# Optimization experiments

Hardware: AMD Instinct MI355X
Metric: run time of the kernel (lower is better)

Reference implementation:

```python
import jax, jax.numpy as jnp
import numpy as np

NUM_HEADS = 8
OUT_CH = 64
IN_CH = 512
N_NODES = 65536


def setup_inputs() -> dict:
    key = jax.random.key(0)
    ks = jax.random.split(key, 8)
    s = 1.0 / np.sqrt(IN_CH)
    return {
        "query_input": jax.random.normal(ks[0], (N_NODES, IN_CH), jnp.float32),
        "source_input": jax.random.normal(ks[1], (N_NODES, IN_CH), jnp.float32),
        "Wq_w": jax.random.normal(ks[2], (NUM_HEADS * OUT_CH, IN_CH), jnp.float32) * s,
        "Wq_b": jax.random.normal(ks[3], (NUM_HEADS * OUT_CH,), jnp.float32) * s,
        "Wk_w": jax.random.normal(ks[4], (NUM_HEADS * OUT_CH, IN_CH), jnp.float32) * s,
        "Wk_b": jax.random.normal(ks[5], (NUM_HEADS * OUT_CH,), jnp.float32) * s,
        "Wv_w": jax.random.normal(ks[6], (NUM_HEADS * OUT_CH, IN_CH), jnp.float32) * s,
        "Wv_b": jax.random.normal(ks[7], (NUM_HEADS * OUT_CH,), jnp.float32) * s,
    }


def reference(query_input, source_input, Wq_w, Wq_b, Wk_w, Wk_b, Wv_w, Wv_b):
    N = query_input.shape[0]
    # Linear projections (torch nn.Linear: x @ W^T + b), reshape to [N, H, D]
    qs = (query_input @ Wq_w.T + Wq_b).reshape(N, NUM_HEADS, OUT_CH)
    ks = (source_input @ Wk_w.T + Wk_b).reshape(N, NUM_HEADS, OUT_CH)
    vs = (source_input @ Wv_w.T + Wv_b).reshape(N, NUM_HEADS, OUT_CH)
    # GLOBAL Frobenius-norm normalization (torch.norm with no dim)
    qs = qs / jnp.linalg.norm(qs)
    ks = ks / jnp.linalg.norm(ks)
    Nf = jnp.asarray(N, qs.dtype)
    # Global KV aggregation: [H, D, D]
    kvs = jnp.einsum('lhm,lhd->hmd', ks, vs)
    attention_num = jnp.einsum('nhm,hmd->nhd', qs, kvs) + Nf * vs
    ks_sum = ks.sum(axis=0)  # [H, D]
    attention_normalizer = jnp.einsum('nhm,hm->nh', qs, ks_sum)[..., None] + Nf
    attn_output = attention_num / attention_normalizer  # [N, H, D]
    return attn_output.mean(axis=1)  # [N, D]
```

## Files before the change

kernel.cpp:

```cpp
#include <hip/hip_runtime.h>
#include <stdint.h>

typedef __attribute__((ext_vector_type(8))) short short8;
typedef __attribute__((ext_vector_type(4))) float f32x4;

__device__ __forceinline__ uint32_t pk2bf(float a, float b) {
  uint32_t r;
  asm("v_cvt_pk_bf16_f32 %0, %1, %2" : "=v"(r) : "v"(a), "v"(b));
  return r;
}
__device__ __forceinline__ uint16_t f2bf(float a) {
  uint32_t ua = __builtin_bit_cast(uint32_t, a);
  return (uint16_t)((ua + 0x7FFFu + ((ua >> 16) & 1u)) >> 16);
}
__device__ __forceinline__ float bflo(uint32_t w) { return __builtin_bit_cast(float, w << 16); }
__device__ __forceinline__ float bfhi(uint32_t w) { return __builtin_bit_cast(float, w & 0xFFFF0000u); }

__device__ __forceinline__ void gload_lds16(const void* g, void* l) {
  __builtin_amdgcn_global_load_lds(
      (const __attribute__((address_space(1))) uint32_t*)g,
      (__attribute__((address_space(3))) uint32_t*)l, 16, 0, 0);
}

__global__ __launch_bounds__(256) void k_cvtw(const float* __restrict__ Wq,
                                              const float* __restrict__ Wk,
                                              const float* __restrict__ Wv,
                                              uint16_t* __restrict__ Wb) {
  const int idx = blockIdx.x * 256 + threadIdx.x;
  const int sel = idx >> 16;
  const int e = idx & 65535;
  const float* src = (sel == 0) ? Wq : (sel == 1) ? Wk : Wv;
  const float4 v = *(const float4*)(src + (size_t)e * 4);
  uint2 p;
  p.x = pk2bf(v.x, v.y);
  p.y = pk2bf(v.z, v.w);
  *(uint2*)(Wb + (size_t)sel * 262144 + (size_t)e * 4) = p;
}

__global__ __launch_bounds__(256, 2) void k_gemm_qkv(
    const float* __restrict__ qin, const float* __restrict__ sin_,
    const uint16_t* __restrict__ Wb,
    const float* __restrict__ bq, const float* __restrict__ bk,
    const float* __restrict__ bv,
    uint16_t* __restrict__ Qb, uint16_t* __restrict__ Kb, uint16_t* __restrict__ Vb,
    float* __restrict__ norms, float* __restrict__ ks_sum) {
  __shared__ float Asf[128 * 64];
  __shared__ uint16_t Bs[256 * 64];
  __shared__ float ksp[256];
  __shared__ float red[4];

  const int b0 = blockIdx.x;
  const int blk = (b0 & 7) * 384 + (b0 >> 3);
  const int rt = blk / 6, rem = blk % 6;
  const int proj = rem >> 1, ct = rem & 1;
  const int row0 = rt * 128, cb = ct * 256;

  const float* A = proj ? sin_ : qin;
  const uint16_t* W = Wb + (size_t)proj * 262144;
  const float* Bi = (proj == 0) ? bq : (proj == 1) ? bk : bv;
  uint16_t* O = (proj == 0) ? Qb : (proj == 1) ? Kb : Vb;

  const int tid = threadIdx.x;
  const int lane = tid & 63;
  const int wv = tid >> 6;
  const int wr = wv >> 1, wc = wv & 1;
  const int l15 = lane & 15, lhi = lane >> 4;

  f32x4 acc[4][8];
#pragma unroll
  for (int m = 0; m < 4; ++m)
#pragma unroll
    for (int n = 0; n < 8; ++n) acc[m][n] = (f32x4){0.f, 0.f, 0.f, 0.f};

  for (int kt = 0; kt < 8; ++kt) {
    const int k0 = kt * 64;
#pragma unroll
    for (int i = 0; i < 8; ++i) {
      const int arow = (wv * 8 + i) * 4 + (lane >> 4);
      const int ac16 = (lane & 15) ^ (arow & 7);
      gload_lds16(A + (size_t)(row0 + arow) * 512 + k0 + ac16 * 4,
                  &Asf[(wv * 8 + i) * 256]);
    }
#pragma unroll
    for (int i = 0; i < 8; ++i) {
      const int brow = (wv * 8 + i) * 8 + (lane >> 3);
      const int bc16 = (lane & 7) ^ (brow & 7);
      gload_lds16(W + (size_t)(cb + brow) * 512 + k0 + bc16 * 8,
                  &Bs[(wv * 8 + i) * 512]);
    }
    __syncthreads();
#pragma unroll
    for (int kk = 0; kk < 2; ++kk) {
      short8 a[4], b[8];
#pragma unroll
      for (int m = 0; m < 4; ++m) {
        const int r = wr * 64 + m * 16 + l15;
        const int base = r * 256 + kk * 128 + lhi * 32;
        const int sw = (r & 7) << 4;
        const f32x4 f0 = *(const f32x4*)((const char*)Asf + (base ^ sw));
        const f32x4 f1 = *(const f32x4*)((const char*)Asf + ((base + 16) ^ sw));
        uint32_t* ap = (uint32_t*)&a[m];
        ap[0] = pk2bf(f0[0], f0[1]);
        ap[1] = pk2bf(f0[2], f0[3]);
        ap[2] = pk2bf(f1[0], f1[1]);
        ap[3] = pk2bf(f1[2], f1[3]);
      }
#pragma unroll
      for (int n = 0; n < 8; ++n) {
        const int c = wc * 128 + n * 16 + l15;
        const int bo = (c * 128 + kk * 64 + lhi * 16) ^ ((c & 7) << 4);
        b[n] = *(const short8*)((const char*)Bs + bo);
      }
#pragma unroll
      for (int m = 0; m < 4; ++m)
#pragma unroll
        for (int n = 0; n < 8; ++n)
          acc[m][n] = __builtin_amdgcn_mfma_f32_16x16x32_bf16(a[m], b[n], acc[m][n], 0, 0, 0);
    }
    __syncthreads();
  }

  float nrm = 0.f;
  float cs[8];
#pragma unroll
  for (int n = 0; n < 8; ++n) cs[n] = 0.f;
#pragma unroll
  for (int n = 0; n < 8; ++n) {
    const int colg = cb + wc * 128 + n * 16 + l15;
    const float bias = Bi[colg];
#pragma unroll
    for (int m = 0; m < 4; ++m) {
      const int rowb = row0 + wr * 64 + m * 16 + lhi * 4;
#pragma unroll
      for (int r = 0; r < 4; ++r) {
        const float v = acc[m][n][r] + bias;
        O[(size_t)(rowb + r) * 512 + colg] = f2bf(v);
        nrm += v * v;
        cs[n] += v;
      }
    }
  }
#pragma unroll
  for (int o = 32; o >= 1; o >>= 1) nrm += __shfl_xor(nrm, o, 64);
  if (lane == 0) red[wv] = nrm;
  ksp[tid] = 0.f;
  __syncthreads();
  if (proj == 1) {
#pragma unroll
    for (int n = 0; n < 8; ++n) {
      cs[n] += __shfl_xor(cs[n], 16, 64);
      cs[n] += __shfl_xor(cs[n], 32, 64);
    }
    if (lhi == 0) {
#pragma unroll
      for (int n = 0; n < 8; ++n) atomicAdd(&ksp[wc * 128 + n * 16 + l15], cs[n]);
    }
  }
  __syncthreads();
  if (tid == 0 && proj < 2)
    atomicAdd(&norms[proj], red[0] + red[1] + red[2] + red[3]);
  if (proj == 1) atomicAdd(&ks_sum[cb + tid], ksp[tid]);
}

__global__ __launch_bounds__(512) void k_kvs(const uint16_t* __restrict__ Kb,
                                             const uint16_t* __restrict__ Vb,
                                             float* __restrict__ part) {
  __shared__ uint16_t Ks[64 * 128];
  __shared__ uint16_t Vs[64 * 128];
  const int tid = threadIdx.x;
  const int hp = blockIdx.x & 3;
  const int chunk = blockIdx.x >> 2;
  const int tm = tid >> 4, td = tid & 15;
  const int vb = (tm >> 4) * 64;
  float acc[4][4];
#pragma unroll
  for (int a = 0; a < 4; ++a)
#pragma unroll
    for (int b = 0; b < 4; ++b) acc[a][b] = 0.f;

  for (int nb = 0; nb < 8; ++nb) {
    const int n0 = chunk * 512 + nb * 64;
#pragma unroll
    for (int i = 0; i < 2; ++i) {
      const int id = i * 512 + tid;
      const int row = id >> 4, c8 = id & 15;
      *(uint4*)(&Ks[row * 128 + c8 * 8]) =
          *(const uint4*)(Kb + (size_t)(n0 + row) * 512 + hp * 128 + c8 * 8);
      *(uint4*)(&Vs[row * 128 + c8 * 8]) =
          *(const uint4*)(Vb + (size_t)(n0 + row) * 512 + hp * 128 + c8 * 8);
    }
    __syncthreads();
    for (int nn = 0; nn < 64; ++nn) {
      const uint2 kw = *(const uint2*)(&Ks[nn * 128 + tm * 4]);
      const uint2 vw = *(const uint2*)(&Vs[nn * 128 + vb + td * 4]);
      const float km[4] = {bflo(kw.x), bfhi(kw.x), bflo(kw.y), bfhi(kw.y)};
      const float vd[4] = {bflo(vw.x), bfhi(vw.x), bflo(vw.y), bfhi(vw.y)};
#pragma unroll
      for (int a = 0; a < 4; ++a)
#pragma unroll
        for (int b = 0; b < 4; ++b) acc[a][b] = fmaf(km[a], vd[b], acc[a][b]);
    }
    __syncthreads();
  }
  float* p = part + (size_t)chunk * 32768 + (size_t)hp * 128 * 64;
#pragma unroll
  for (int a = 0; a < 4; ++a)
#pragma unroll
    for (int b = 0; b < 4; ++b)
      p[(tm * 4 + a) * 64 + td * 4 + b] = acc[a][b];
}

__global__ __launch_bounds__(256) void k_kvsT(const float* __restrict__ part,
                                              uint16_t* __restrict__ kvsT) {
  const int id = blockIdx.x * 256 + threadIdx.x;
  const int k = id >> 6, d = id & 63;
  float s0 = 0.f, s1 = 0.f, s2 = 0.f, s3 = 0.f;
#pragma unroll
  for (int c = 0; c < 128; c += 4) {
    s0 += part[(size_t)(c + 0) * 32768 + id];
    s1 += part[(size_t)(c + 1) * 32768 + id];
    s2 += part[(size_t)(c + 2) * 32768 + id];
    s3 += part[(size_t)(c + 3) * 32768 + id];
  }
  kvsT[(size_t)d * 512 + k] = f2bf((s0 + s1) + (s2 + s3));
}

__global__ __launch_bounds__(256, 2) void k_num(const uint16_t* __restrict__ Qb,
                                                const uint16_t* __restrict__ Vb,
                                                const uint16_t* __restrict__ kvsT,
                                                const float* __restrict__ ks_sum,
                                                const float* __restrict__ norms,
                                                float* __restrict__ out) {
  __shared__ uint16_t KT[64 * 512];
  __shared__ float kss[512];
  __shared__ float aS[128 * 8];
  __shared__ float bS[128 * 8];
  const int tid = threadIdx.x, lane = tid & 63, wv = tid >> 6;
  const int l15 = lane & 15, lhi = lane >> 4;
  const int row0 = blockIdx.x * 128;

#pragma unroll
  for (int i = 0; i < 16; ++i) {
    const int d = wv * 16 + i;
    const int sc = lane ^ (d & 7);
    gload_lds16(kvsT + (size_t)d * 512 + sc * 8, &KT[d * 512]);
  }
  kss[tid] = ks_sum[tid];
  kss[tid + 256] = ks_sum[tid + 256];
  __syncthreads();
  const float scale = 1.0f / (sqrtf(norms[0]) * sqrtf(norms[1]));

  {
    const int r = tid >> 1, h0 = (tid & 1) * 4;
#pragma unroll
    for (int hh = 0; hh < 4; ++hh) {
      const int h = h0 + hh;
      const uint16_t* q = Qb + (size_t)(row0 + r) * 512 + h * 64;
      const float* ks = &kss[h * 64];
      float dot = 0.f;
#pragma unroll
      for (int i = 0; i < 8; ++i) {
        const uint4 w = *(const uint4*)(q + i * 8);
        const uint32_t dw[4] = {w.x, w.y, w.z, w.w};
#pragma unroll
        for (int c = 0; c < 4; ++c) {
          dot = fmaf(bflo(dw[c]), ks[i * 8 + c * 2], dot);
          dot = fmaf(bfhi(dw[c]), ks[i * 8 + c * 2 + 1], dot);
        }
      }
      const float den = fmaf(scale, dot, 65536.0f);
      aS[r * 8 + h] = scale / (8.0f * den);
      bS[r * 8 + h] = 8192.0f / den;
    }
  }
  __syncthreads();

  short8 If[2][4];
#pragma unroll
  for (int kk = 0; kk < 2; ++kk)
#pragma unroll
    for (int n = 0; n < 4; ++n) {
      const int pos = n * 16 + l15 - kk * 32 - lhi * 8;
      uint32_t* p = (uint32_t*)&If[kk][n];
#pragma unroll
      for (int jw = 0; jw < 4; ++jw)
        p[jw] = ((pos >> 1) == jw) ? ((pos & 1) ? 0x3F800000u : 0x00003F80u) : 0u;
    }

  f32x4 acc[2][4];
#pragma unroll
  for (int m = 0; m < 2; ++m)
#pragma unroll
    for (int n = 0; n < 4; ++n) acc[m][n] = (f32x4){0.f, 0.f, 0.f, 0.f};

  for (int h = 0; h < 8; ++h) {
#pragma unroll
    for (int kk = 0; kk < 2; ++kk) {
      short8 bfr[4];
#pragma unroll
      for (int n = 0; n < 4; ++n) {
        const int d = n * 16 + l15;
        const int bo = (d * 1024 + h * 128 + kk * 64 + lhi * 16) ^ ((d & 7) << 4);
        bfr[n] = *(const short8*)((const char*)KT + bo);
      }
#pragma unroll
      for (int m = 0; m < 2; ++m) {
        const int r = wv * 32 + m * 16 + l15;
        const float sc = aS[r * 8 + h];
        const uint4 w =
            *(const uint4*)(Qb + (size_t)(row0 + r) * 512 + h * 64 + kk * 32 + lhi * 8);
        const uint32_t dw[4] = {w.x, w.y, w.z, w.w};
        short8 af;
        uint32_t* ap = (uint32_t*)&af;
#pragma unroll
        for (int c = 0; c < 4; ++c) ap[c] = pk2bf(bflo(dw[c]) * sc, bfhi(dw[c]) * sc);
#pragma unroll
        for (int n = 0; n < 4; ++n)
          acc[m][n] = __builtin_amdgcn_mfma_f32_16x16x32_bf16(af, bfr[n], acc[m][n], 0, 0, 0);
      }
    }
  }
  for (int h = 0; h < 8; ++h) {
#pragma unroll
    for (int kk = 0; kk < 2; ++kk) {
#pragma unroll
      for (int m = 0; m < 2; ++m) {
        const int r = wv * 32 + m * 16 + l15;
        const float sc = bS[r * 8 + h];
        const uint4 w =
            *(const uint4*)(Vb + (size_t)(row0 + r) * 512 + h * 64 + kk * 32 + lhi * 8);
        const uint32_t dw[4] = {w.x, w.y, w.z, w.w};
        short8 af;
        uint32_t* ap = (uint32_t*)&af;
#pragma unroll
        for (int c = 0; c < 4; ++c) ap[c] = pk2bf(bflo(dw[c]) * sc, bfhi(dw[c]) * sc);
#pragma unroll
        for (int n = 0; n < 4; ++n)
          acc[m][n] = __builtin_amdgcn_mfma_f32_16x16x32_bf16(af, If[kk][n], acc[m][n], 0, 0, 0);
      }
    }
  }

#pragma unroll
  for (int m = 0; m < 2; ++m)
#pragma unroll
    for (int n = 0; n < 4; ++n)
#pragma unroll
      for (int j = 0; j < 4; ++j)
        out[(size_t)(row0 + wv * 32 + m * 16 + lhi * 4 + j) * 64 + n * 16 + l15] =
            acc[m][n][j];
}

extern "C" void kernel_launch(void* const* d_in, const int* in_sizes, int n_in,
                              void* d_out, int out_size, void* d_ws, size_t ws_size,
                              hipStream_t stream) {
  const float* qin = (const float*)d_in[0];
  const float* sin_ = (const float*)d_in[1];
  const float* Wq = (const float*)d_in[2];
  const float* bq = (const float*)d_in[3];
  const float* Wk = (const float*)d_in[4];
  const float* bk = (const float*)d_in[5];
  const float* Wv = (const float*)d_in[6];
  const float* bv = (const float*)d_in[7];
  float* out = (float*)d_out;

  char* ws = (char*)d_ws;
  float* ks_sum = (float*)ws;
  float* norms = (float*)(ws + 2048);
  uint16_t* kvsT = (uint16_t*)(ws + 4096);
  uint16_t* Wb = (uint16_t*)(ws + 69632);
  uint16_t* Qb = (uint16_t*)(ws + (2ull << 20));
  uint16_t* Kb = (uint16_t*)(ws + (2ull << 20) + 67108864ull);
  uint16_t* Vb = (uint16_t*)(ws + (2ull << 20) + 134217728ull);
  float* part = (float*)(ws + 194ull * 1048576ull);

  hipMemsetAsync(d_ws, 0, 2056, stream);

  k_cvtw<<<dim3(768), dim3(256), 0, stream>>>(Wq, Wk, Wv, Wb);
  k_gemm_qkv<<<dim3(3072), dim3(256), 0, stream>>>(qin, sin_, Wb, bq, bk, bv,
                                                   Qb, Kb, Vb, norms, ks_sum);
  k_kvs<<<dim3(512), dim3(512), 0, stream>>>(Kb, Vb, part);
  k_kvsT<<<dim3(128), dim3(256), 0, stream>>>(part, kvsT);
  k_num<<<dim3(512), dim3(256), 0, stream>>>(Qb, Vb, kvsT, ks_sum, norms, out);
}
```

Measured before the change: 299.5 us.

## Fuse normalizer dot into main head loop and merge Q/V passes

Removes the separate prologue that computed per-row, per-head normalizer scales into shared memory, along with its barrier. The Q·ks_sum dot product is now computed inside the head loop from the same Q fragments the MFMA path loads, with shuffles reducing across lanes. The Q and V passes are merged into one loop over heads. This avoids reading Q from global memory twice and frees the aS/bS shared arrays. In exchange it adds more registers per thread and puts a reciprocal plus shuffles on each head iteration.

```diff
diff --git a/kernel.cpp b/kernel.cpp
--- a/kernel.cpp
+++ b/kernel.cpp
@@ -233,8 +233,6 @@
                                                 float* __restrict__ out) {
   __shared__ uint16_t KT[64 * 512];
   __shared__ float kss[512];
-  __shared__ float aS[128 * 8];
-  __shared__ float bS[128 * 8];
   const int tid = threadIdx.x, lane = tid & 63, wv = tid >> 6;
   const int l15 = lane & 15, lhi = lane >> 4;
   const int row0 = blockIdx.x * 128;
@@ -250,31 +248,6 @@
   __syncthreads();
   const float scale = 1.0f / (sqrtf(norms[0]) * sqrtf(norms[1]));
 
-  {
-    const int r = tid >> 1, h0 = (tid & 1) * 4;
-#pragma unroll
-    for (int hh = 0; hh < 4; ++hh) {
-      const int h = h0 + hh;
-      const uint16_t* q = Qb + (size_t)(row0 + r) * 512 + h * 64;
-      const float* ks = &kss[h * 64];
-      float dot = 0.f;
-#pragma unroll
-      for (int i = 0; i < 8; ++i) {
-        const uint4 w = *(const uint4*)(q + i * 8);
-        const uint32_t dw[4] = {w.x, w.y, w.z, w.w};
-#pragma unroll
-        for (int c = 0; c < 4; ++c) {
-          dot = fmaf(bflo(dw[c]), ks[i * 8 + c * 2], dot);
-          dot = fmaf(bfhi(dw[c]), ks[i * 8 + c * 2 + 1], dot);
-        }
-      }
-      const float den = fmaf(scale, dot, 65536.0f);
-      aS[r * 8 + h] = scale / (8.0f * den);
-      bS[r * 8 + h] = 8192.0f / den;
-    }
-  }
-  __syncthreads();
-
   short8 If[2][4];
 #pragma unroll
   for (int kk = 0; kk < 2; ++kk)
@@ -294,6 +267,43 @@
     for (int n = 0; n < 4; ++n) acc[m][n] = (f32x4){0.f, 0.f, 0.f, 0.f};
 
   for (int h = 0; h < 8; ++h) {
+    uint4 wq[2][2], wvv[2][2];
+#pragma unroll
+    for (int m = 0; m < 2; ++m) {
+      const int r = row0 + wv * 32 + m * 16 + l15;
+#pragma unroll
+      for (int kk = 0; kk < 2; ++kk) {
+        wq[m][kk] = *(const uint4*)(Qb + (size_t)r * 512 + h * 64 + kk * 32 + lhi * 8);
+        wvv[m][kk] = *(const uint4*)(Vb + (size_t)r * 512 + h * 64 + kk * 32 + lhi * 8);
+      }
+    }
+    f32x4 ks0[2], ks1[2];
+#pragma unroll
+    for (int kk = 0; kk < 2; ++kk) {
+      const float* kp = &kss[h * 64 + kk * 32 + lhi * 8];
+      ks0[kk] = *(const f32x4*)kp;
+      ks1[kk] = *(const f32x4*)(kp + 4);
+    }
+    float rden[2];
+#pragma unroll
+    for (int m = 0; m < 2; ++m) {
+      float d = 0.f;
+#pragma unroll
+      for (int kk = 0; kk < 2; ++kk) {
+        const uint32_t dw[4] = {wq[m][kk].x, wq[m][kk].y, wq[m][kk].z, wq[m][kk].w};
+        d = fmaf(bflo(dw[0]), ks0[kk][0], d);
+        d = fmaf(bfhi(dw[0]), ks0[kk][1], d);
+        d = fmaf(bflo(dw[1]), ks0[kk][2], d);
+        d = fmaf(bfhi(dw[1]), ks0[kk][3], d);
+        d = fmaf(bflo(dw[2]), ks1[kk][0], d);
+        d = fmaf(bfhi(dw[2]), ks1[kk][1], d);
+        d = fmaf(bflo(dw[3]), ks1[kk][2], d);
+        d = fmaf(bfhi(dw[3]), ks1[kk][3], d);
+      }
+      d += __shfl_xor(d, 16, 64);
+      d += __shfl_xor(d, 32, 64);
+      rden[m] = 1.0f / fmaf(scale, d, 65536.0f);
+    }
 #pragma unroll
     for (int kk = 0; kk < 2; ++kk) {
       short8 bfr[4];
@@ -305,38 +315,24 @@
       }
 #pragma unroll
       for (int m = 0; m < 2; ++m) {
-        const int r = wv * 32 + m * 16 + l15;
-        const float sc = aS[r * 8 + h];
-        const uint4 w =
-            *(const uint4*)(Qb + (size_t)(row0 + r) * 512 + h * 64 + kk * 32 + lhi * 8);
-        const uint32_t dw[4] = {w.x, w.y, w.z, w.w};
-        short8 af;
+        const float a_s = scale * 0.125f * rden[m];
+        const float b_s = 8192.0f * rden[m];
+        const uint32_t dq[4] = {wq[m][kk].x, wq[m][kk].y, wq[m][kk].z, wq[m][kk].w};
+        const uint32_t dv[4] = {wvv[m][kk].x, wvv[m][kk].y, wvv[m][kk].z, wvv[m][kk].w};
+        short8 af, vf;
         uint32_t* ap = (uint32_t*)&af;
-#pragma unroll
-        for (int c = 0; c < 4; ++c) ap[c] = pk2bf(bflo(dw[c]) * sc, bfhi(dw[c]) * sc);
+        uint32_t* vp = (uint32_t*)&vf;
+#pragma unroll
+        for (int c = 0; c < 4; ++c) {
+          ap[c] = pk2bf(bflo(dq[c]) * a_s, bfhi(dq[c]) * a_s);
+          vp[c] = pk2bf(bflo(dv[c]) * b_s, bfhi(dv[c]) * b_s);
+        }
 #pragma unroll
         for (int n = 0; n < 4; ++n)
           acc[m][n] = __builtin_amdgcn_mfma_f32_16x16x32_bf16(af, bfr[n], acc[m][n], 0, 0, 0);
-      }
-    }
-  }
-  for (int h = 0; h < 8; ++h) {
-#pragma unroll
-    for (int kk = 0; kk < 2; ++kk) {
-#pragma unroll
-      for (int m = 0; m < 2; ++m) {
-        const int r = wv * 32 + m * 16 + l15;
-        const float sc = bS[r * 8 + h];
-        const uint4 w =
-            *(const uint4*)(Vb + (size_t)(row0 + r) * 512 + h * 64 + kk * 32 + lhi * 8);
-        const uint32_t dw[4] = {w.x, w.y, w.z, w.w};
-        short8 af;
-        uint32_t* ap = (uint32_t*)&af;
-#pragma unroll
-        for (int c = 0; c < 4; ++c) ap[c] = pk2bf(bflo(dw[c]) * sc, bfhi(dw[c]) * sc);
 #pragma unroll
         for (int n = 0; n < 4; ++n)
-          acc[m][n] = __builtin_amdgcn_mfma_f32_16x16x32_bf16(af, If[kk][n], acc[m][n], 0, 0, 0);
+          acc[m][n] = __builtin_amdgcn_mfma_f32_16x16x32_bf16(vf, If[kk][n], acc[m][n], 0, 0, 0);
       }
     }
   }
```

After: 288.7 us (median of 2 runs). 3.6% less time.
